# Optimization experiments

Measured on AMD Instinct MI355X. Metric: run time of the kernel, lower is better.

## Reference

```python
import jax, jax.numpy as jnp
import numpy as np

B, S, D = 8, 4096, 64
SQRT_DIM = float(np.sqrt(D))

def setup_inputs() -> dict:
    key = jax.random.key(0)
    kq, kk, kv, km = jax.random.split(key, 4)
    query = jax.random.normal(kq, (B, S, D), dtype=jnp.float32)
    k_ = jax.random.normal(kk, (B, S, D), dtype=jnp.float32)
    v_ = jax.random.normal(kv, (B, S, D), dtype=jnp.float32)
    mask = jax.random.randint(km, (B, S, S), 0, 2).astype(bool)
    return {"query": query, "key": k_, "value": v_, "mask": mask}

def reference(query, key, value, mask):
    # score: [B, S_q, S_k]
    score = jnp.einsum('bqd,bkd->bqk', query, key) / SQRT_DIM
    score = jnp.where(mask, jnp.float32(-10000.0), score)
    attn = jax.nn.softmax(score, axis=-1)
    context = jnp.einsum('bqk,bkd->bqd', attn, value)
    return (context, attn)
```

## Files before the change

### kernel.cpp

```cpp
#include <hip/hip_runtime.h>
#include <hip/hip_bf16.h>

#define BB 8
#define SS 4096
#define DD 64
#define QT 64
#define KTILE 128
#define NKT (SS / KTILE)
#define NTHREADS 512

typedef __attribute__((ext_vector_type(4))) short short4v;
typedef __attribute__((ext_vector_type(8))) short short8v;
typedef __attribute__((ext_vector_type(4))) float float4v;

__device__ __forceinline__ unsigned short f2bf(float f) {
  union { __hip_bfloat16 b; unsigned short u; } cv;
  cv.b = __float2bfloat16(f);
  return cv.u;
}

__device__ __forceinline__ short8v load8(const unsigned short* p) {
  union { short4v h[2]; short8v v; } u;
  u.h[0] = *(const short4v*)p;
  u.h[1] = *(const short4v*)(p + 4);
  return u.v;
}

__global__ __launch_bounds__(NTHREADS, 2)
void attn_fused_kernel(const float* __restrict__ Q, const float* __restrict__ K,
                       const float* __restrict__ V, const int* __restrict__ M,
                       float* __restrict__ Octx, float* __restrict__ Oattn) {
  __shared__ __align__(16) unsigned short Qs[QT][72];
  __shared__ __align__(16) unsigned short Ks[KTILE][72];
  __shared__ __align__(16) unsigned short Vt[DD][KTILE + 8];
  __shared__ __align__(16) unsigned short Ps[QT][KTILE + 8];
  __shared__ unsigned long long Bm[QT * 65];
  __shared__ float RowSum[QT];
  __shared__ float InvRow[QT];

  const int tid  = threadIdx.x;
  const int w    = tid >> 6;
  const int lane = tid & 63;
  const int quad = lane >> 4;
  const int l15  = lane & 15;
  const int qs   = (w & 3) << 4;
  const int kh   = (w >> 2) << 6;
  const int dh   = (w >> 2) << 5;

  const int bb = blockIdx.x & 7;
  const int qt = blockIdx.x >> 3;
  const int q0 = qt * QT;

  const float* Qg = Q + ((size_t)bb * SS + q0) * DD;
  const float* Kg = K + (size_t)bb * SS * DD;
  const float* Vg = V + (size_t)bb * SS * DD;
  const int*   Mg = M + ((size_t)bb * SS + q0) * (size_t)SS;
  float* Ag = Oattn + ((size_t)bb * SS + q0) * (size_t)SS;
  float* Cg = Octx + ((size_t)bb * SS + q0) * DD;

  if (tid < QT) RowSum[tid] = 0.f;

  for (int i = tid; i < QT * 16; i += NTHREADS) {
    const int r = i >> 4, c4 = (i & 15) << 2;
    const float4 qv = *(const float4*)(Qg + (size_t)r * DD + c4);
    short4v pk;
    pk.x = (short)f2bf(qv.x); pk.y = (short)f2bf(qv.y);
    pk.z = (short)f2bf(qv.z); pk.w = (short)f2bf(qv.w);
    *(short4v*)&Qs[r][c4] = pk;
  }

  for (int it = w; it < QT * 16; it += 8) {
    const int r = it >> 4, g = it & 15;
    const int4 m4 = *(const int4*)(Mg + (size_t)r * SS + g * 256 + lane * 4);
    const unsigned long long b0 = __ballot(m4.x != 0);
    const unsigned long long b1 = __ballot(m4.y != 0);
    const unsigned long long b2 = __ballot(m4.z != 0);
    const unsigned long long b3 = __ballot(m4.w != 0);
    if (lane == 0) {
      unsigned long long* dst = &Bm[r * 65 + (g << 2)];
      dst[0] = b0; dst[1] = b1; dst[2] = b2; dst[3] = b3;
    }
  }
  __syncthreads();

  const short8v aq0 = load8(&Qs[qs + l15][quad * 8]);
  const short8v aq1 = load8(&Qs[qs + l15][32 + quad * 8]);

  float rsum[4] = {0.f, 0.f, 0.f, 0.f};
  for (int kt = 0; kt < NKT; ++kt) {
    for (int i = tid; i < KTILE * 16; i += NTHREADS) {
      const int r = i >> 4, c4 = (i & 15) << 2;
      const float4 kv = *(const float4*)(Kg + (size_t)(kt * KTILE + r) * DD + c4);
      short4v pk;
      pk.x = (short)f2bf(kv.x); pk.y = (short)f2bf(kv.y);
      pk.z = (short)f2bf(kv.z); pk.w = (short)f2bf(kv.w);
      *(short4v*)&Ks[r][c4] = pk;
    }
    __syncthreads();
#pragma unroll
    for (int t = 0; t < 4; ++t) {
      float4v acc = {0.f, 0.f, 0.f, 0.f};
      const unsigned short* kp = &Ks[kh + t * 16 + l15][quad * 8];
      const short8v b0 = load8(kp);
      const short8v b1 = load8(kp + 32);
      acc = __builtin_amdgcn_mfma_f32_16x16x32_bf16(aq0, b0, acc, 0, 0, 0);
      acc = __builtin_amdgcn_mfma_f32_16x16x32_bf16(aq1, b1, acc, 0, 0, 0);
      const int c = kt * KTILE + kh + t * 16 + l15;
      const int widx = ((c >> 8) << 2) + (c & 3);
      const int bit = (c >> 2) & 63;
#pragma unroll
      for (int r = 0; r < 4; ++r) {
        const int row = qs + quad * 4 + r;
        const bool msk = (Bm[row * 65 + widx] >> bit) & 1ULL;
        const float p = msk ? 0.f : __expf(acc[r] * 0.125f);
        rsum[r] += p;
      }
    }
    __syncthreads();
  }

#pragma unroll
  for (int r = 0; r < 4; ++r) {
    float v = rsum[r];
    v += __shfl_xor(v, 1);
    v += __shfl_xor(v, 2);
    v += __shfl_xor(v, 4);
    v += __shfl_xor(v, 8);
    if (l15 == 0) atomicAdd(&RowSum[qs + quad * 4 + r], v);
  }
  __syncthreads();
  if (tid < QT) {
    const float s = RowSum[tid];
    InvRow[tid] = (s != 0.f) ? 1.f / s : 0.f;
  }
  __syncthreads();
  float inv[4];
#pragma unroll
  for (int r = 0; r < 4; ++r) inv[r] = InvRow[qs + quad * 4 + r];

  float4v cacc0 = {0.f, 0.f, 0.f, 0.f}, cacc1 = {0.f, 0.f, 0.f, 0.f};
  for (int kt = 0; kt < NKT; ++kt) {
    for (int i = tid; i < KTILE * 16; i += NTHREADS) {
      const int r = i >> 4, c4 = (i & 15) << 2;
      const float4 kv = *(const float4*)(Kg + (size_t)(kt * KTILE + r) * DD + c4);
      short4v pk;
      pk.x = (short)f2bf(kv.x); pk.y = (short)f2bf(kv.y);
      pk.z = (short)f2bf(kv.z); pk.w = (short)f2bf(kv.w);
      *(short4v*)&Ks[r][c4] = pk;
    }
    {
      const int kk = tid & 127;
      const int d0 = (tid >> 7) << 4;
#pragma unroll
      for (int c4 = 0; c4 < 4; ++c4) {
        const float4 vv = *(const float4*)(Vg + (size_t)(kt * KTILE + kk) * DD + d0 + c4 * 4);
        Vt[d0 + c4 * 4 + 0][kk] = f2bf(vv.x);
        Vt[d0 + c4 * 4 + 1][kk] = f2bf(vv.y);
        Vt[d0 + c4 * 4 + 2][kk] = f2bf(vv.z);
        Vt[d0 + c4 * 4 + 3][kk] = f2bf(vv.w);
      }
    }
    __syncthreads();
#pragma unroll
    for (int t = 0; t < 4; ++t) {
      float4v acc = {0.f, 0.f, 0.f, 0.f};
      const unsigned short* kp = &Ks[kh + t * 16 + l15][quad * 8];
      const short8v b0 = load8(kp);
      const short8v b1 = load8(kp + 32);
      acc = __builtin_amdgcn_mfma_f32_16x16x32_bf16(aq0, b0, acc, 0, 0, 0);
      acc = __builtin_amdgcn_mfma_f32_16x16x32_bf16(aq1, b1, acc, 0, 0, 0);
      const int c = kt * KTILE + kh + t * 16 + l15;
      const int widx = ((c >> 8) << 2) + (c & 3);
      const int bit = (c >> 2) & 63;
#pragma unroll
      for (int r = 0; r < 4; ++r) {
        const int row = qs + quad * 4 + r;
        const bool msk = (Bm[row * 65 + widx] >> bit) & 1ULL;
        const float p = msk ? 0.f : __expf(acc[r] * 0.125f);
        Ps[row][kh + t * 16 + l15] = f2bf(p);
        Ag[(size_t)row * SS + c] = p * inv[r];
      }
    }
    __syncthreads();
#pragma unroll
    for (int ks = 0; ks < 4; ++ks) {
      const short8v ap = *(const short8v*)&Ps[qs + l15][ks * 32 + quad * 8];
      const short8v bv0 = *(const short8v*)&Vt[dh + l15][ks * 32 + quad * 8];
      const short8v bv1 = *(const short8v*)&Vt[dh + 16 + l15][ks * 32 + quad * 8];
      cacc0 = __builtin_amdgcn_mfma_f32_16x16x32_bf16(ap, bv0, cacc0, 0, 0, 0);
      cacc1 = __builtin_amdgcn_mfma_f32_16x16x32_bf16(ap, bv1, cacc1, 0, 0, 0);
    }
    __syncthreads();
  }

#pragma unroll
  for (int r = 0; r < 4; ++r) {
    const int row = qs + quad * 4 + r;
    Cg[(size_t)row * DD + dh + l15] = cacc0[r] * inv[r];
    Cg[(size_t)row * DD + dh + 16 + l15] = cacc1[r] * inv[r];
  }
}

extern "C" void kernel_launch(void* const* d_in, const int* in_sizes, int n_in,
                              void* d_out, int out_size, void* d_ws, size_t ws_size,
                              hipStream_t stream) {
  const float* q = (const float*)d_in[0];
  const float* k = (const float*)d_in[1];
  const float* v = (const float*)d_in[2];
  const int*   m = (const int*)d_in[3];
  float* ctx  = (float*)d_out;
  float* attn = (float*)d_out + (size_t)BB * SS * DD;
  dim3 grid(BB * (SS / QT));
  attn_fused_kernel<<<grid, NTHREADS, 0, stream>>>(q, k, v, m, ctx, attn);
}
```

Before: 1.290 ms.

## Repack mask bits into registers and alias mask LDS with V/P buffers

Each thread now extracts its own mask bits from the shared ballot bitmap once, before the main loops, and keeps them in registers. This removes the per-element LDS loads of 64-bit mask words in both passes. The freed bitmap storage is aliased with the Vt and Ps buffers in one pooled LDS array, and the launch bound is raised from 2 to 4 blocks per CU to increase occupancy. The register-held masks add pressure that may conflict with the higher occupancy target.

```diff
diff --git a/kernel.cpp b/kernel.cpp
--- a/kernel.cpp
+++ b/kernel.cpp
@@ -26,17 +26,20 @@
   return u.v;
 }
 
-__global__ __launch_bounds__(NTHREADS, 2)
+__global__ __launch_bounds__(NTHREADS, 4)
 void attn_fused_kernel(const float* __restrict__ Q, const float* __restrict__ K,
                        const float* __restrict__ V, const int* __restrict__ M,
                        float* __restrict__ Octx, float* __restrict__ Oattn) {
   __shared__ __align__(16) unsigned short Qs[QT][72];
   __shared__ __align__(16) unsigned short Ks[KTILE][72];
-  __shared__ __align__(16) unsigned short Vt[DD][KTILE + 8];
-  __shared__ __align__(16) unsigned short Ps[QT][KTILE + 8];
-  __shared__ unsigned long long Bm[QT * 65];
+  __shared__ __align__(16) unsigned char Pool[(DD + QT) * (KTILE + 8) * 2];
   __shared__ float RowSum[QT];
   __shared__ float InvRow[QT];
+
+  unsigned long long* Bm = (unsigned long long*)Pool;
+  typedef unsigned short PRow[KTILE + 8];
+  PRow* Vt = (PRow*)Pool;
+  PRow* Ps = (PRow*)(Pool + (size_t)DD * (KTILE + 8) * 2);
 
   const int tid  = threadIdx.x;
   const int w    = tid >> 6;
@@ -86,37 +89,58 @@
   const short8v aq0 = load8(&Qs[qs + l15][quad * 8]);
   const short8v aq1 = load8(&Qs[qs + l15][32 + quad * 8]);
 
+  const int B0 = (kh >> 2) + (l15 >> 2);
+  unsigned long long mreg[4][2];
+#pragma unroll
+  for (int r = 0; r < 4; ++r) {
+    const int row = qs + quad * 4 + r;
+#pragma unroll
+    for (int h = 0; h < 2; ++h) {
+      unsigned long long acc = 0ULL;
+#pragma unroll
+      for (int g8 = 0; g8 < 8; ++g8) {
+        const int w16 = h * 8 + g8;
+        const unsigned long long W = Bm[row * 65 + w16 * 4 + (l15 & 3)] >> B0;
+        const unsigned nl = ((((unsigned)W & 0x1111u) * 0x1248u) >> 12) & 0xFu;
+        const unsigned nh = ((((unsigned)(W >> 32) & 0x1111u) * 0x1248u) >> 12) & 0xFu;
+        acc |= (unsigned long long)(nl | (nh << 4)) << (g8 * 8);
+      }
+      mreg[r][h] = acc;
+    }
+  }
+
   float rsum[4] = {0.f, 0.f, 0.f, 0.f};
-  for (int kt = 0; kt < NKT; ++kt) {
-    for (int i = tid; i < KTILE * 16; i += NTHREADS) {
-      const int r = i >> 4, c4 = (i & 15) << 2;
-      const float4 kv = *(const float4*)(Kg + (size_t)(kt * KTILE + r) * DD + c4);
-      short4v pk;
-      pk.x = (short)f2bf(kv.x); pk.y = (short)f2bf(kv.y);
-      pk.z = (short)f2bf(kv.z); pk.w = (short)f2bf(kv.w);
-      *(short4v*)&Ks[r][c4] = pk;
-    }
-    __syncthreads();
-#pragma unroll
-    for (int t = 0; t < 4; ++t) {
-      float4v acc = {0.f, 0.f, 0.f, 0.f};
-      const unsigned short* kp = &Ks[kh + t * 16 + l15][quad * 8];
-      const short8v b0 = load8(kp);
-      const short8v b1 = load8(kp + 32);
-      acc = __builtin_amdgcn_mfma_f32_16x16x32_bf16(aq0, b0, acc, 0, 0, 0);
-      acc = __builtin_amdgcn_mfma_f32_16x16x32_bf16(aq1, b1, acc, 0, 0, 0);
-      const int c = kt * KTILE + kh + t * 16 + l15;
-      const int widx = ((c >> 8) << 2) + (c & 3);
-      const int bit = (c >> 2) & 63;
-#pragma unroll
-      for (int r = 0; r < 4; ++r) {
-        const int row = qs + quad * 4 + r;
-        const bool msk = (Bm[row * 65 + widx] >> bit) & 1ULL;
-        const float p = msk ? 0.f : __expf(acc[r] * 0.125f);
-        rsum[r] += p;
-      }
-    }
-    __syncthreads();
+#pragma unroll
+  for (int half = 0; half < 2; ++half) {
+    for (int kt2 = 0; kt2 < 16; ++kt2) {
+      const int kt = (half << 4) | kt2;
+      for (int i = tid; i < KTILE * 16; i += NTHREADS) {
+        const int r = i >> 4, c4 = (i & 15) << 2;
+        const float4 kv = *(const float4*)(Kg + (size_t)(kt * KTILE + r) * DD + c4);
+        short4v pk;
+        pk.x = (short)f2bf(kv.x); pk.y = (short)f2bf(kv.y);
+        pk.z = (short)f2bf(kv.z); pk.w = (short)f2bf(kv.w);
+        *(short4v*)&Ks[r][c4] = pk;
+      }
+      __syncthreads();
+#pragma unroll
+      for (int t = 0; t < 4; ++t) {
+        float4v acc = {0.f, 0.f, 0.f, 0.f};
+        const unsigned short* kp = &Ks[kh + t * 16 + l15][quad * 8];
+        const short8v b0 = load8(kp);
+        const short8v b1 = load8(kp + 32);
+        acc = __builtin_amdgcn_mfma_f32_16x16x32_bf16(aq0, b0, acc, 0, 0, 0);
+        acc = __builtin_amdgcn_mfma_f32_16x16x32_bf16(aq1, b1, acc, 0, 0, 0);
+        const int bsh = ((kt2 >> 1) << 3) | ((kt2 & 1) << 2) | t;
+#pragma unroll
+        for (int r = 0; r < 4; ++r) {
+          const bool msk = (mreg[r][half] >> bsh) & 1ULL;
+          const float p = msk ? 0.f : __expf(acc[r] * 0.125f);
+          rsum[r] += p;
+        }
+      }
+      __syncthreads();
+    }
   }
 
 #pragma unroll
@@ -139,58 +163,61 @@
   for (int r = 0; r < 4; ++r) inv[r] = InvRow[qs + quad * 4 + r];
 
   float4v cacc0 = {0.f, 0.f, 0.f, 0.f}, cacc1 = {0.f, 0.f, 0.f, 0.f};
-  for (int kt = 0; kt < NKT; ++kt) {
-    for (int i = tid; i < KTILE * 16; i += NTHREADS) {
-      const int r = i >> 4, c4 = (i & 15) << 2;
-      const float4 kv = *(const float4*)(Kg + (size_t)(kt * KTILE + r) * DD + c4);
-      short4v pk;
-      pk.x = (short)f2bf(kv.x); pk.y = (short)f2bf(kv.y);
-      pk.z = (short)f2bf(kv.z); pk.w = (short)f2bf(kv.w);
-      *(short4v*)&Ks[r][c4] = pk;
-    }
-    {
-      const int kk = tid & 127;
-      const int d0 = (tid >> 7) << 4;
-#pragma unroll
-      for (int c4 = 0; c4 < 4; ++c4) {
-        const float4 vv = *(const float4*)(Vg + (size_t)(kt * KTILE + kk) * DD + d0 + c4 * 4);
-        Vt[d0 + c4 * 4 + 0][kk] = f2bf(vv.x);
-        Vt[d0 + c4 * 4 + 1][kk] = f2bf(vv.y);
-        Vt[d0 + c4 * 4 + 2][kk] = f2bf(vv.z);
-        Vt[d0 + c4 * 4 + 3][kk] = f2bf(vv.w);
-      }
-    }
-    __syncthreads();
-#pragma unroll
-    for (int t = 0; t < 4; ++t) {
-      float4v acc = {0.f, 0.f, 0.f, 0.f};
-      const unsigned short* kp = &Ks[kh + t * 16 + l15][quad * 8];
-      const short8v b0 = load8(kp);
-      const short8v b1 = load8(kp + 32);
-      acc = __builtin_amdgcn_mfma_f32_16x16x32_bf16(aq0, b0, acc, 0, 0, 0);
-      acc = __builtin_amdgcn_mfma_f32_16x16x32_bf16(aq1, b1, acc, 0, 0, 0);
-      const int c = kt * KTILE + kh + t * 16 + l15;
-      const int widx = ((c >> 8) << 2) + (c & 3);
-      const int bit = (c >> 2) & 63;
-#pragma unroll
-      for (int r = 0; r < 4; ++r) {
-        const int row = qs + quad * 4 + r;
-        const bool msk = (Bm[row * 65 + widx] >> bit) & 1ULL;
-        const float p = msk ? 0.f : __expf(acc[r] * 0.125f);
-        Ps[row][kh + t * 16 + l15] = f2bf(p);
-        Ag[(size_t)row * SS + c] = p * inv[r];
-      }
-    }
-    __syncthreads();
-#pragma unroll
-    for (int ks = 0; ks < 4; ++ks) {
-      const short8v ap = *(const short8v*)&Ps[qs + l15][ks * 32 + quad * 8];
-      const short8v bv0 = *(const short8v*)&Vt[dh + l15][ks * 32 + quad * 8];
-      const short8v bv1 = *(const short8v*)&Vt[dh + 16 + l15][ks * 32 + quad * 8];
-      cacc0 = __builtin_amdgcn_mfma_f32_16x16x32_bf16(ap, bv0, cacc0, 0, 0, 0);
-      cacc1 = __builtin_amdgcn_mfma_f32_16x16x32_bf16(ap, bv1, cacc1, 0, 0, 0);
-    }
-    __syncthreads();
+#pragma unroll
+  for (int half = 0; half < 2; ++half) {
+    for (int kt2 = 0; kt2 < 16; ++kt2) {
+      const int kt = (half << 4) | kt2;
+      for (int i = tid; i < KTILE * 16; i += NTHREADS) {
+        const int r = i >> 4, c4 = (i & 15) << 2;
+        const float4 kv = *(const float4*)(Kg + (size_t)(kt * KTILE + r) * DD + c4);
+        short4v pk;
+        pk.x = (short)f2bf(kv.x); pk.y = (short)f2bf(kv.y);
+        pk.z = (short)f2bf(kv.z); pk.w = (short)f2bf(kv.w);
+        *(short4v*)&Ks[r][c4] = pk;
+      }
+      {
+        const int kk = tid & 127;
+        const int d0 = (tid >> 7) << 4;
+#pragma unroll
+        for (int c4 = 0; c4 < 4; ++c4) {
+          const float4 vv = *(const float4*)(Vg + (size_t)(kt * KTILE + kk) * DD + d0 + c4 * 4);
+          Vt[d0 + c4 * 4 + 0][kk] = f2bf(vv.x);
+          Vt[d0 + c4 * 4 + 1][kk] = f2bf(vv.y);
+          Vt[d0 + c4 * 4 + 2][kk] = f2bf(vv.z);
+          Vt[d0 + c4 * 4 + 3][kk] = f2bf(vv.w);
+        }
+      }
+      __syncthreads();
+#pragma unroll
+      for (int t = 0; t < 4; ++t) {
+        float4v acc = {0.f, 0.f, 0.f, 0.f};
+        const unsigned short* kp = &Ks[kh + t * 16 + l15][quad * 8];
+        const short8v b0 = load8(kp);
+        const short8v b1 = load8(kp + 32);
+        acc = __builtin_amdgcn_mfma_f32_16x16x32_bf16(aq0, b0, acc, 0, 0, 0);
+        acc = __builtin_amdgcn_mfma_f32_16x16x32_bf16(aq1, b1, acc, 0, 0, 0);
+        const int c = kt * KTILE + kh + t * 16 + l15;
+        const int bsh = ((kt2 >> 1) << 3) | ((kt2 & 1) << 2) | t;
+#pragma unroll
+        for (int r = 0; r < 4; ++r) {
+          const int row = qs + quad * 4 + r;
+          const bool msk = (mreg[r][half] >> bsh) & 1ULL;
+          const float p = msk ? 0.f : __expf(acc[r] * 0.125f);
+          Ps[row][kh + t * 16 + l15] = f2bf(p);
+          Ag[(size_t)row * SS + c] = p * inv[r];
+        }
+      }
+      __syncthreads();
+#pragma unroll
+      for (int ks = 0; ks < 4; ++ks) {
+        const short8v ap = *(const short8v*)&Ps[qs + l15][ks * 32 + quad * 8];
+        const short8v bv0 = *(const short8v*)&Vt[dh + l15][ks * 32 + quad * 8];
+        const short8v bv1 = *(const short8v*)&Vt[dh + 16 + l15][ks * 32 + quad * 8];
+        cacc0 = __builtin_amdgcn_mfma_f32_16x16x32_bf16(ap, bv0, cacc0, 0, 0, 0);
+        cacc1 = __builtin_amdgcn_mfma_f32_16x16x32_bf16(ap, bv1, cacc1, 0, 0, 0);
+      }
+      __syncthreads();
+    }
   }
 
 #pragma unroll
```

After: 1.100 ms. 1.17x faster.

## Halve query and key tiles, double-buffer K, and cache mask bits in registers

Applied to the files above, without the earlier changes.

Shrinks the query tile to 32 and the key tile to 64 so more blocks fit per CU, and aliases the LDS buffers into one pool. K tiles are now double-buffered: the next tile is loaded from global memory while MFMAs on the current tile run, leaving one barrier per iteration. Each thread also gathers its mask bits once into 64-bit registers, replacing per-element LDS bitmask lookups. The trade-offs are twice as many blocks, each re-reading K and V, and more intricate indexing.

```diff
diff --git a/kernel.cpp b/kernel.cpp
--- a/kernel.cpp
+++ b/kernel.cpp
@@ -4,8 +4,8 @@
 #define BB 8
 #define SS 4096
 #define DD 64
-#define QT 64
-#define KTILE 128
+#define QT 32
+#define KTILE 64
 #define NKT (SS / KTILE)
 #define NTHREADS 512
 
@@ -19,33 +19,37 @@
   return cv.u;
 }
 
-__device__ __forceinline__ short8v load8(const unsigned short* p) {
-  union { short4v h[2]; short8v v; } u;
-  u.h[0] = *(const short4v*)p;
-  u.h[1] = *(const short4v*)(p + 4);
-  return u.v;
-}
-
-__global__ __launch_bounds__(NTHREADS, 2)
+__device__ __forceinline__ short4v pack4(const float4 v) {
+  short4v p;
+  p.x = (short)f2bf(v.x); p.y = (short)f2bf(v.y);
+  p.z = (short)f2bf(v.z); p.w = (short)f2bf(v.w);
+  return p;
+}
+
+__global__ __launch_bounds__(NTHREADS, 8)
 void attn_fused_kernel(const float* __restrict__ Q, const float* __restrict__ K,
                        const float* __restrict__ V, const int* __restrict__ M,
                        float* __restrict__ Octx, float* __restrict__ Oattn) {
   __shared__ __align__(16) unsigned short Qs[QT][72];
-  __shared__ __align__(16) unsigned short Ks[KTILE][72];
-  __shared__ __align__(16) unsigned short Vt[DD][KTILE + 8];
-  __shared__ __align__(16) unsigned short Ps[QT][KTILE + 8];
-  __shared__ unsigned long long Bm[QT * 65];
+  __shared__ __align__(16) unsigned char Pool[32256];
   __shared__ float RowSum[QT];
   __shared__ float InvRow[QT];
+
+  typedef unsigned short Row72[72];
+  Row72* Ks0 = (Row72*)Pool;
+  Row72* Ks1 = (Row72*)(Pool + 9216);
+  Row72* Vt  = (Row72*)(Pool + 18432);
+  Row72* Ps  = (Row72*)(Pool + 27648);
+  unsigned long long* Bm = (unsigned long long*)Pool;
 
   const int tid  = threadIdx.x;
   const int w    = tid >> 6;
   const int lane = tid & 63;
   const int quad = lane >> 4;
   const int l15  = lane & 15;
-  const int qs   = (w & 3) << 4;
-  const int kh   = (w >> 2) << 6;
-  const int dh   = (w >> 2) << 5;
+  const int qs   = (w & 1) << 4;
+  const int kq   = (w >> 1) << 4;
+  const int dq   = (w >> 1) << 4;
 
   const int bb = blockIdx.x & 7;
   const int qt = blockIdx.x >> 3;
@@ -60,16 +64,19 @@
 
   if (tid < QT) RowSum[tid] = 0.f;
 
-  for (int i = tid; i < QT * 16; i += NTHREADS) {
-    const int r = i >> 4, c4 = (i & 15) << 2;
-    const float4 qv = *(const float4*)(Qg + (size_t)r * DD + c4);
-    short4v pk;
-    pk.x = (short)f2bf(qv.x); pk.y = (short)f2bf(qv.y);
-    pk.z = (short)f2bf(qv.z); pk.w = (short)f2bf(qv.w);
-    *(short4v*)&Qs[r][c4] = pk;
-  }
-
-  for (int it = w; it < QT * 16; it += 8) {
+  const int rK = tid >> 4, cK = (tid & 15) << 2;
+
+  const float4 pk0A = *(const float4*)(Kg + (size_t)rK * DD + cK);
+  const float4 pk0B = *(const float4*)(Kg + (size_t)(32 + rK) * DD + cK);
+
+  {
+    const float4 qv = *(const float4*)(Qg + (size_t)rK * DD + cK);
+    *(short4v*)&Qs[rK][cK] = pack4(qv);
+  }
+
+#pragma unroll 4
+  for (int j = 0; j < 64; ++j) {
+    const int it = (j << 3) | w;
     const int r = it >> 4, g = it & 15;
     const int4 m4 = *(const int4*)(Mg + (size_t)r * SS + g * 256 + lane * 4);
     const unsigned long long b0 = __ballot(m4.x != 0);
@@ -83,50 +90,62 @@
   }
   __syncthreads();
 
-  const short8v aq0 = load8(&Qs[qs + l15][quad * 8]);
-  const short8v aq1 = load8(&Qs[qs + l15][32 + quad * 8]);
+  const short8v aq0 = *(const short8v*)&Qs[qs + l15][quad * 8];
+  const short8v aq1 = *(const short8v*)&Qs[qs + l15][32 + quad * 8];
+
+  const int B0 = (kq >> 2) + (l15 >> 2);
+  unsigned long long mreg[4];
+#pragma unroll
+  for (int rr = 0; rr < 4; ++rr) {
+    const int row = qs + quad * 4 + rr;
+    unsigned long long acc = 0ULL;
+#pragma unroll
+    for (int w16 = 0; w16 < 16; ++w16) {
+      unsigned long long x = Bm[row * 65 + (w16 << 2) + (l15 & 3)] >> B0;
+      x &= 0x0001000100010001ULL;
+      x |= x >> 15;
+      x |= x >> 30;
+      acc |= (x & 0xFULL) << (w16 << 2);
+    }
+    mreg[rr] = acc;
+  }
+  __syncthreads();
+
+  *(short4v*)&Ks0[rK][cK] = pack4(pk0A);
+  *(short4v*)&Ks0[rK + 32][cK] = pack4(pk0B);
+  __syncthreads();
 
   float rsum[4] = {0.f, 0.f, 0.f, 0.f};
   for (int kt = 0; kt < NKT; ++kt) {
-    for (int i = tid; i < KTILE * 16; i += NTHREADS) {
-      const int r = i >> 4, c4 = (i & 15) << 2;
-      const float4 kv = *(const float4*)(Kg + (size_t)(kt * KTILE + r) * DD + c4);
-      short4v pk;
-      pk.x = (short)f2bf(kv.x); pk.y = (short)f2bf(kv.y);
-      pk.z = (short)f2bf(kv.z); pk.w = (short)f2bf(kv.w);
-      *(short4v*)&Ks[r][c4] = pk;
-    }
+    Row72* Kc = (kt & 1) ? Ks1 : Ks0;
+    Row72* Kn = (kt & 1) ? Ks0 : Ks1;
+    const int ktn = (kt + 1) & (NKT - 1);
+    const float4 kA = *(const float4*)(Kg + (size_t)(ktn * KTILE + rK) * DD + cK);
+    const float4 kB = *(const float4*)(Kg + (size_t)(ktn * KTILE + 32 + rK) * DD + cK);
+    const short8v b0 = *(const short8v*)&Kc[kq + l15][quad * 8];
+    const short8v b1 = *(const short8v*)&Kc[kq + l15][32 + quad * 8];
+    float4v acc = {0.f, 0.f, 0.f, 0.f};
+    acc = __builtin_amdgcn_mfma_f32_16x16x32_bf16(aq0, b0, acc, 0, 0, 0);
+    acc = __builtin_amdgcn_mfma_f32_16x16x32_bf16(aq1, b1, acc, 0, 0, 0);
+#pragma unroll
+    for (int rr = 0; rr < 4; ++rr) {
+      const bool msk = (mreg[rr] >> kt) & 1ULL;
+      const float p = msk ? 0.f : __expf(acc[rr] * 0.125f);
+      rsum[rr] += p;
+    }
+    *(short4v*)&Kn[rK][cK] = pack4(kA);
+    *(short4v*)&Kn[rK + 32][cK] = pack4(kB);
     __syncthreads();
-#pragma unroll
-    for (int t = 0; t < 4; ++t) {
-      float4v acc = {0.f, 0.f, 0.f, 0.f};
-      const unsigned short* kp = &Ks[kh + t * 16 + l15][quad * 8];
-      const short8v b0 = load8(kp);
-      const short8v b1 = load8(kp + 32);
-      acc = __builtin_amdgcn_mfma_f32_16x16x32_bf16(aq0, b0, acc, 0, 0, 0);
-      acc = __builtin_amdgcn_mfma_f32_16x16x32_bf16(aq1, b1, acc, 0, 0, 0);
-      const int c = kt * KTILE + kh + t * 16 + l15;
-      const int widx = ((c >> 8) << 2) + (c & 3);
-      const int bit = (c >> 2) & 63;
-#pragma unroll
-      for (int r = 0; r < 4; ++r) {
-        const int row = qs + quad * 4 + r;
-        const bool msk = (Bm[row * 65 + widx] >> bit) & 1ULL;
-        const float p = msk ? 0.f : __expf(acc[r] * 0.125f);
-        rsum[r] += p;
-      }
-    }
-    __syncthreads();
-  }
-
-#pragma unroll
-  for (int r = 0; r < 4; ++r) {
-    float v = rsum[r];
+  }
+
+#pragma unroll
+  for (int rr = 0; rr < 4; ++rr) {
+    float v = rsum[rr];
     v += __shfl_xor(v, 1);
     v += __shfl_xor(v, 2);
     v += __shfl_xor(v, 4);
     v += __shfl_xor(v, 8);
-    if (l15 == 0) atomicAdd(&RowSum[qs + quad * 4 + r], v);
+    if (l15 == 0) atomicAdd(&RowSum[qs + quad * 4 + rr], v);
   }
   __syncthreads();
   if (tid < QT) {
@@ -136,68 +155,55 @@
   __syncthreads();
   float inv[4];
 #pragma unroll
-  for (int r = 0; r < 4; ++r) inv[r] = InvRow[qs + quad * 4 + r];
-
-  float4v cacc0 = {0.f, 0.f, 0.f, 0.f}, cacc1 = {0.f, 0.f, 0.f, 0.f};
+  for (int rr = 0; rr < 4; ++rr) inv[rr] = InvRow[qs + quad * 4 + rr];
+
+  float4v cacc = {0.f, 0.f, 0.f, 0.f};
+  const int d0 = w << 3;
   for (int kt = 0; kt < NKT; ++kt) {
-    for (int i = tid; i < KTILE * 16; i += NTHREADS) {
-      const int r = i >> 4, c4 = (i & 15) << 2;
-      const float4 kv = *(const float4*)(Kg + (size_t)(kt * KTILE + r) * DD + c4);
-      short4v pk;
-      pk.x = (short)f2bf(kv.x); pk.y = (short)f2bf(kv.y);
-      pk.z = (short)f2bf(kv.z); pk.w = (short)f2bf(kv.w);
-      *(short4v*)&Ks[r][c4] = pk;
-    }
-    {
-      const int kk = tid & 127;
-      const int d0 = (tid >> 7) << 4;
-#pragma unroll
-      for (int c4 = 0; c4 < 4; ++c4) {
-        const float4 vv = *(const float4*)(Vg + (size_t)(kt * KTILE + kk) * DD + d0 + c4 * 4);
-        Vt[d0 + c4 * 4 + 0][kk] = f2bf(vv.x);
-        Vt[d0 + c4 * 4 + 1][kk] = f2bf(vv.y);
-        Vt[d0 + c4 * 4 + 2][kk] = f2bf(vv.z);
-        Vt[d0 + c4 * 4 + 3][kk] = f2bf(vv.w);
-      }
-    }
+    Row72* Kc = (kt & 1) ? Ks1 : Ks0;
+    Row72* Kn = (kt & 1) ? Ks0 : Ks1;
+    const int ktn = (kt + 1) & (NKT - 1);
+    const float4 vA = *(const float4*)(Vg + (size_t)(kt * KTILE + lane) * DD + d0);
+    const float4 vB = *(const float4*)(Vg + (size_t)(kt * KTILE + lane) * DD + d0 + 4);
+    const float4 kA = *(const float4*)(Kg + (size_t)(ktn * KTILE + rK) * DD + cK);
+    const float4 kB = *(const float4*)(Kg + (size_t)(ktn * KTILE + 32 + rK) * DD + cK);
+    const short8v b0 = *(const short8v*)&Kc[kq + l15][quad * 8];
+    const short8v b1 = *(const short8v*)&Kc[kq + l15][32 + quad * 8];
+    float4v acc = {0.f, 0.f, 0.f, 0.f};
+    acc = __builtin_amdgcn_mfma_f32_16x16x32_bf16(aq0, b0, acc, 0, 0, 0);
+    acc = __builtin_amdgcn_mfma_f32_16x16x32_bf16(aq1, b1, acc, 0, 0, 0);
+#pragma unroll
+    for (int rr = 0; rr < 4; ++rr) {
+      const int row = qs + quad * 4 + rr;
+      const bool msk = (mreg[rr] >> kt) & 1ULL;
+      const float p = msk ? 0.f : __expf(acc[rr] * 0.125f);
+      Ps[row][kq + l15] = f2bf(p);
+      Ag[(size_t)row * SS + kt * KTILE + kq + l15] = p * inv[rr];
+    }
+    Vt[d0 + 0][lane] = f2bf(vA.x);
+    Vt[d0 + 1][lane] = f2bf(vA.y);
+    Vt[d0 + 2][lane] = f2bf(vA.z);
+    Vt[d0 + 3][lane] = f2bf(vA.w);
+    Vt[d0 + 4][lane] = f2bf(vB.x);
+    Vt[d0 + 5][lane] = f2bf(vB.y);
+    Vt[d0 + 6][lane] = f2bf(vB.z);
+    Vt[d0 + 7][lane] = f2bf(vB.w);
     __syncthreads();
 #pragma unroll
-    for (int t = 0; t < 4; ++t) {
-      float4v acc = {0.f, 0.f, 0.f, 0.f};
-      const unsigned short* kp = &Ks[kh + t * 16 + l15][quad * 8];
-      const short8v b0 = load8(kp);
-      const short8v b1 = load8(kp + 32);
-      acc = __builtin_amdgcn_mfma_f32_16x16x32_bf16(aq0, b0, acc, 0, 0, 0);
-      acc = __builtin_amdgcn_mfma_f32_16x16x32_bf16(aq1, b1, acc, 0, 0, 0);
-      const int c = kt * KTILE + kh + t * 16 + l15;
-      const int widx = ((c >> 8) << 2) + (c & 3);
-      const int bit = (c >> 2) & 63;
-#pragma unroll
-      for (int r = 0; r < 4; ++r) {
-        const int row = qs + quad * 4 + r;
-        const bool msk = (Bm[row * 65 + widx] >> bit) & 1ULL;
-        const float p = msk ? 0.f : __expf(acc[r] * 0.125f);
-        Ps[row][kh + t * 16 + l15] = f2bf(p);
-        Ag[(size_t)row * SS + c] = p * inv[r];
-      }
-    }
+    for (int ks = 0; ks < 2; ++ks) {
+      const short8v ap = *(const short8v*)&Ps[qs + l15][ks * 32 + quad * 8];
+      const short8v bv = *(const short8v*)&Vt[dq + l15][ks * 32 + quad * 8];
+      cacc = __builtin_amdgcn_mfma_f32_16x16x32_bf16(ap, bv, cacc, 0, 0, 0);
+    }
+    *(short4v*)&Kn[rK][cK] = pack4(kA);
+    *(short4v*)&Kn[rK + 32][cK] = pack4(kB);
     __syncthreads();
-#pragma unroll
-    for (int ks = 0; ks < 4; ++ks) {
-      const short8v ap = *(const short8v*)&Ps[qs + l15][ks * 32 + quad * 8];
-      const short8v bv0 = *(const short8v*)&Vt[dh + l15][ks * 32 + quad * 8];
-      const short8v bv1 = *(const short8v*)&Vt[dh + 16 + l15][ks * 32 + quad * 8];
-      cacc0 = __builtin_amdgcn_mfma_f32_16x16x32_bf16(ap, bv0, cacc0, 0, 0, 0);
-      cacc1 = __builtin_amdgcn_mfma_f32_16x16x32_bf16(ap, bv1, cacc1, 0, 0, 0);
-    }
-    __syncthreads();
-  }
-
-#pragma unroll
-  for (int r = 0; r < 4; ++r) {
-    const int row = qs + quad * 4 + r;
-    Cg[(size_t)row * DD + dh + l15] = cacc0[r] * inv[r];
-    Cg[(size_t)row * DD + dh + 16 + l15] = cacc1[r] * inv[r];
+  }
+
+#pragma unroll
+  for (int rr = 0; rr < 4; ++rr) {
+    const int row = qs + quad * 4 + rr;
+    Cg[(size_t)row * DD + dq + l15] = cacc[rr] * inv[rr];
   }
 }
 
```

Result: faster. 1.128 ms (-12.5%).
